# Kernel optimization log

Hardware: AMD Instinct MI355X
Metric: run time of the kernel (lower is better)

## Reference

```python
import jax, jax.numpy as jnp
import numpy as np

B, M, N, D = 16, 1024, 1024, 512
DIST_THRESH = 0.3
NUM_SINK = 8


def setup_inputs() -> dict:
    key = jax.random.key(0)
    k1, k2, k3, k4 = jax.random.split(key, 4)
    return {
        "tra_feats": jax.random.normal(k1, (B, M, D), jnp.float32),
        "det_feats": jax.random.normal(k2, (B, N, D), jnp.float32),
        "tra_loc": jax.random.uniform(k3, (B, M, 2), jnp.float32),
        "det_loc": jax.random.uniform(k4, (B, N, 2), jnp.float32),
        "alpha": jnp.ones((1,), jnp.float32),
        "eplison": jnp.zeros((1,), jnp.float32),
    }


def _sinkhorn(C, log_a, log_b, lambd, num_sink):
    # log-domain unrolled Sinkhorn: P_ij = exp(log_p), marginals a (rows), b (cols)
    log_p = -C / lambd
    def step(lp, _):
        lp = lp - (jax.nn.logsumexp(lp, axis=-1, keepdims=True) - log_a[:, None])
        lp = lp - (jax.nn.logsumexp(lp, axis=-2, keepdims=True) - log_b[None, :])
        return lp, None
    log_p, _ = jax.lax.scan(step, log_p, None, length=num_sink)
    # final row normalization (standard unrolled-sinkhorn convention)
    log_p = log_p - (jax.nn.logsumexp(log_p, axis=-1, keepdims=True) - log_a[:, None])
    return jnp.exp(log_p)


def _per_graph(tf, df, tl, dl, alpha, lambd):
    n1 = jnp.linalg.norm(tf, axis=-1, keepdims=True)          # [M,1]
    n2 = jnp.linalg.norm(df, axis=-1, keepdims=True)          # [N,1]
    d2 = jnp.sum((tl[:, None, :] - dl[None, :, :]) ** 2, -1)  # [M,N] squared cdist
    mask = (jnp.sqrt(d2) <= DIST_THRESH).astype(tf.dtype)
    corr = (tf @ df.T) / (n1 * n2.T) * mask                   # masked cosine similarity
    m, n = corr.shape
    # augment with dustbin row/col filled with learnable alpha
    top = jnp.concatenate([corr, jnp.full((m, 1), alpha, corr.dtype)], axis=1)
    bot = jnp.full((1, n + 1), alpha, corr.dtype)
    couplings = jnp.concatenate([top, bot], axis=0)           # [M+1, N+1]
    norm = 1.0 / (m + n)
    a_aug = jnp.full((m + 1,), norm, corr.dtype).at[-1].set(norm * n)
    b_aug = jnp.full((n + 1,), norm, corr.dtype).at[-1].set(norm * m)
    p = _sinkhorn(1.0 - couplings, jnp.log(a_aug), jnp.log(b_aug), lambd, NUM_SINK)
    return p * (m + n)


def reference(tra_feats, det_feats, tra_loc, det_loc, alpha, eplison):
    a = alpha[0]
    lambd = jnp.exp(eplison[0]) + 0.03
    f = jax.vmap(lambda tf, df, tl, dl: _per_graph(tf, df, tl, dl, a, lambd))
    return f(tra_feats, det_feats, tra_loc, det_loc)   # [B, M+1, N+1]
```

## Files before the change

### kernel.cpp

```cpp
#include <hip/hip_runtime.h>
#include <math.h>

#define B_ 16
#define M_ 1024
#define N_ 1024
#define D_ 512
#define MP1 1025
#define NP1 1025
#define NUM_SINK 8
#define BK 64
#define SSTR 1024
#define VSTR 1028
#define LOG_NORM (-7.6246189861593985f)
#define LOG_HALF (-0.6931471805599453f)

typedef __attribute__((ext_vector_type(8))) short bf16x8;
typedef __attribute__((ext_vector_type(4))) float f32x4;
typedef __attribute__((ext_vector_type(8))) _Float16 h16x8;

__device__ inline short f2bf(float x) {
    unsigned u = __builtin_bit_cast(unsigned, x);
    u = (u + 0x7FFFu + ((u >> 16) & 1u)) >> 16;
    return (short)u;
}

__device__ inline void gload16(const void* g, void* l) {
    __builtin_amdgcn_global_load_lds(
        (const __attribute__((address_space(1))) unsigned int*)g,
        (__attribute__((address_space(3))) unsigned int*)l, 16, 0, 0);
}

template<bool PRE>
__global__ __launch_bounds__(256) void norms_kernel_t(
    const float* __restrict__ tf, const float* __restrict__ df,
    float* __restrict__ inv1, float* __restrict__ inv2,
    unsigned short* __restrict__ tfh, unsigned short* __restrict__ dfh)
{
    int w = (blockIdx.x * 256 + threadIdx.x) >> 6;
    int lane = threadIdx.x & 63;
    if (w >= B_ * 2048) return;
    int b = w >> 11;
    int rr = w & 2047;
    const float* src;
    float* dst = nullptr;
    unsigned short* dsth = nullptr;
    if (rr < M_) { src = tf + ((size_t)b * M_ + rr) * D_;
                   if (!PRE) dst = inv1 + b * M_ + rr;
                   if (PRE)  dsth = tfh + ((size_t)b * M_ + rr) * D_; }
    else         { src = df + ((size_t)b * N_ + (rr - M_)) * D_;
                   if (!PRE) dst = inv2 + b * N_ + (rr - M_);
                   if (PRE)  dsth = dfh + ((size_t)b * N_ + (rr - M_)) * D_; }
    float4 x = *(const float4*)(src + lane * 4);
    float4 y = *(const float4*)(src + 256 + lane * 4);
    float ss = x.x*x.x + x.y*x.y + x.z*x.z + x.w*x.w
             + y.x*y.x + y.y*y.y + y.z*y.z + y.w*y.w;
    #pragma unroll
    for (int o = 32; o; o >>= 1) ss += __shfl_xor(ss, o);
    if (PRE) {
        float rn = rsqrtf(ss);
        ushort4 hx, hy;
        hx.x = (unsigned short)f2bf(x.x*rn); hx.y = (unsigned short)f2bf(x.y*rn);
        hx.z = (unsigned short)f2bf(x.z*rn); hx.w = (unsigned short)f2bf(x.w*rn);
        hy.x = (unsigned short)f2bf(y.x*rn); hy.y = (unsigned short)f2bf(y.y*rn);
        hy.z = (unsigned short)f2bf(y.z*rn); hy.w = (unsigned short)f2bf(y.w*rn);
        *(ushort4*)(dsth + lane * 4) = hx;
        *(ushort4*)(dsth + 256 + lane * 4) = hy;
    } else {
        if (lane == 0) *dst = 1.0f / sqrtf(ss);
    }
}

template<int MODE>
__global__ __launch_bounds__(256) void gemm_s_kernel(
    const void* __restrict__ A, const void* __restrict__ Bm,
    const float* __restrict__ tl, const float* __restrict__ dl,
    const float* __restrict__ inv1, const float* __restrict__ inv2,
    const float* __restrict__ eps_p, void* __restrict__ Sout)
{
    __shared__ __align__(16) unsigned short As[128 * BK];
    __shared__ __align__(16) unsigned short Bs[128 * BK];

    int flat = blockIdx.x;
    int swz = (flat & 7) * 128 + (flat >> 3);
    int jb = swz & 7, ib = (swz >> 3) & 7;
    int b  = swz >> 6;
    int i0 = ib * 128;
    int j0 = jb * 128;

    int tid  = threadIdx.x;
    int lane = tid & 63;
    int w    = tid >> 6;
    int wm   = w >> 1, wn = w & 1;

    f32x4 acc[4][4] = {};

    if constexpr (MODE == 2) {
        const unsigned short* Ah = (const unsigned short*)A  + (size_t)b * M_ * D_;
        const unsigned short* Bh = (const unsigned short*)Bm + (size_t)b * N_ * D_;
        int gcol = ((lane & 7) ^ (lane >> 3)) << 3;
        int rloc = lane >> 3;
        for (int k0 = 0; k0 < D_; k0 += BK) {
            #pragma unroll
            for (int c = 0; c < 4; ++c) {
                int r = (w * 4 + c) * 8 + rloc;
                gload16(Ah + (size_t)(i0 + r) * D_ + k0 + gcol,
                        (char*)As + (w * 4 + c) * 1024 + lane * 16);
                gload16(Bh + (size_t)(j0 + r) * D_ + k0 + gcol,
                        (char*)Bs + (w * 4 + c) * 1024 + lane * 16);
            }
            __syncthreads();
            #pragma unroll
            for (int ks = 0; ks < 2; ++ks) {
                int kb = ks * 64 + ((lane >> 4) << 4);
                bf16x8 af[4], bfr[4];
                #pragma unroll
                for (int m = 0; m < 4; ++m) {
                    int ra = wm * 64 + m * 16 + (lane & 15);
                    af[m] = *(const bf16x8*)((const char*)As + ra * 128 + (kb ^ ((ra & 7) << 4)));
                    int rb = wn * 64 + m * 16 + (lane & 15);
                    bfr[m] = *(const bf16x8*)((const char*)Bs + rb * 128 + (kb ^ ((rb & 7) << 4)));
                }
                #pragma unroll
                for (int m = 0; m < 4; ++m)
                    #pragma unroll
                    for (int n = 0; n < 4; ++n)
                        acc[m][n] = __builtin_amdgcn_mfma_f32_16x16x32_bf16(af[m], bfr[n], acc[m][n], 0, 0, 0);
            }
            __syncthreads();
        }
    } else {
        const float* Ab = (const float*)A  + (size_t)b * M_ * D_;
        const float* Bb = (const float*)Bm + (size_t)b * N_ * D_;
        int seg   = tid & 7;
        int rbase = tid >> 3;
        for (int k0 = 0; k0 < D_; k0 += BK) {
            #pragma unroll
            for (int rr = 0; rr < 4; ++rr) {
                int r = rbase + rr * 32;
                int colx = (seg * 16) ^ ((r & 7) << 4);
                {
                    const float* pa = Ab + (size_t)(i0 + r) * D_ + k0 + seg * 8;
                    float4 a0 = *(const float4*)pa;
                    float4 a1 = *(const float4*)(pa + 4);
                    bf16x8 hv;
                    hv[0] = f2bf(a0.x); hv[1] = f2bf(a0.y); hv[2] = f2bf(a0.z); hv[3] = f2bf(a0.w);
                    hv[4] = f2bf(a1.x); hv[5] = f2bf(a1.y); hv[6] = f2bf(a1.z); hv[7] = f2bf(a1.w);
                    *(bf16x8*)((char*)As + r * 128 + colx) = hv;
                }
                {
                    const float* pb = Bb + (size_t)(j0 + r) * D_ + k0 + seg * 8;
                    float4 b0 = *(const float4*)pb;
                    float4 b1 = *(const float4*)(pb + 4);
                    bf16x8 hv;
                    hv[0] = f2bf(b0.x); hv[1] = f2bf(b0.y); hv[2] = f2bf(b0.z); hv[3] = f2bf(b0.w);
                    hv[4] = f2bf(b1.x); hv[5] = f2bf(b1.y); hv[6] = f2bf(b1.z); hv[7] = f2bf(b1.w);
                    *(bf16x8*)((char*)Bs + r * 128 + colx) = hv;
                }
            }
            __syncthreads();
            #pragma unroll
            for (int ks = 0; ks < 2; ++ks) {
                int kb = ks * 64 + ((lane >> 4) << 4);
                bf16x8 af[4], bfr[4];
                #pragma unroll
                for (int m = 0; m < 4; ++m) {
                    int ra = wm * 64 + m * 16 + (lane & 15);
                    af[m] = *(const bf16x8*)((const char*)As + ra * 128 + (kb ^ ((ra & 7) << 4)));
                    int rb = wn * 64 + m * 16 + (lane & 15);
                    bfr[m] = *(const bf16x8*)((const char*)Bs + rb * 128 + (kb ^ ((rb & 7) << 4)));
                }
                #pragma unroll
                for (int m = 0; m < 4; ++m)
                    #pragma unroll
                    for (int n = 0; n < 4; ++n)
                        acc[m][n] = __builtin_amdgcn_mfma_f32_16x16x32_bf16(af[m], bfr[n], acc[m][n], 0, 0, 0);
            }
            __syncthreads();
        }
    }

    float lam = __expf(eps_p[0]) + 0.03f;
    float inv_lam = 1.0f / lam;
    int crow0 = i0 + wm * 64;
    int ccol0 = j0 + wn * 64;
    int rlane = lane >> 4;
    int clane = lane & 15;

    float invb_[4], dlx_[4], dly_[4];
    #pragma unroll
    for (int n = 0; n < 4; ++n) {
        int j = ccol0 + n * 16 + clane;
        if (MODE != 2) invb_[n] = inv2[b * N_ + j];
        dlx_[n]  = dl[((size_t)b * N_ + j) * 2 + 0];
        dly_[n]  = dl[((size_t)b * N_ + j) * 2 + 1];
    }
    #pragma unroll
    for (int m = 0; m < 4; ++m) {
        #pragma unroll
        for (int reg = 0; reg < 4; ++reg) {
            int i = crow0 + m * 16 + rlane * 4 + reg;
            float inva = (MODE != 2) ? inv1[b * M_ + i] : 1.0f;
            float tlx  = tl[((size_t)b * M_ + i) * 2 + 0];
            float tly  = tl[((size_t)b * M_ + i) * 2 + 1];
            #pragma unroll
            for (int n = 0; n < 4; ++n) {
                float cosv = (MODE == 2) ? acc[m][n][reg]
                                         : acc[m][n][reg] * inva * invb_[n];
                float dx = tlx - dlx_[n];
                float dy = tly - dly_[n];
                float msk = (dx * dx + dy * dy <= 0.09f) ? 1.0f : 0.0f;
                float val = (cosv * msk - 1.0f) * inv_lam;
                int col = ccol0 + n * 16 + clane;
                if (MODE >= 1) {
                    _Float16* Srow = (_Float16*)Sout + ((size_t)b * M_ + i) * SSTR;
                    Srow[col] = (_Float16)val;
                } else {
                    float* Srow = (float*)Sout + ((size_t)b * MP1 + i) * NP1;
                    Srow[col] = val;
                }
            }
        }
    }
}

__global__ __launch_bounds__(256) void init_hv(
    float* __restrict__ v, float* __restrict__ sums_p)
{
    int t = blockIdx.x * 256 + threadIdx.x;
    if (t < B_ * VSTR) v[t] = 0.f;
    int u2 = t - B_ * VSTR;
    if (u2 >= 0 && u2 < 2 * B_ * 17) {
        int p = u2 / (B_ * 17), s = u2 % 17;
        sums_p[u2] = (p == 0 && s == 0) ? 1025.0f : 0.f;
    }
}

__global__ __launch_bounds__(256) void rowcol32(
    const _Float16* __restrict__ Sh, const float* __restrict__ v,
    float* __restrict__ ps,
    const float* __restrict__ alpha_p, const float* __restrict__ eps_p)
{
    int blk = blockIdx.x;
    int b = blk >> 5, k = blk & 31;
    int tid = threadIdx.x, lane = tid & 63, w = tid >> 6;

    __shared__ float red[4][64][17];

    const float* vb = v + (size_t)b * VSTR;
    float vreg[16];
    {
        float4 v0 = *(const float4*)(vb + lane * 8);
        float4 v1 = *(const float4*)(vb + lane * 8 + 4);
        float4 v2 = *(const float4*)(vb + 512 + lane * 8);
        float4 v3 = *(const float4*)(vb + 512 + lane * 8 + 4);
        vreg[0]=v0.x; vreg[1]=v0.y; vreg[2]=v0.z; vreg[3]=v0.w;
        vreg[4]=v1.x; vreg[5]=v1.y; vreg[6]=v1.z; vreg[7]=v1.w;
        vreg[8]=v2.x; vreg[9]=v2.y; vreg[10]=v2.z; vreg[11]=v2.w;
        vreg[12]=v3.x; vreg[13]=v3.y; vreg[14]=v3.z; vreg[15]=v3.w;
    }
    float lam = __expf(eps_p[0]) + 0.03f;
    float s_a = (alpha_p[0] - 1.0f) / lam;
    float et16c = __expf(s_a + vb[1024]);

    const _Float16* Sb = Sh + ((size_t)b << 20);
    int rbase = k * 32 + w * 8;

    float creg[16] = {};
    float sum_scale = 0.f;

    #pragma unroll
    for (int g = 0; g < 2; ++g) {
        h16x8 h0[4], h1[4];
        #pragma unroll
        for (int rr = 0; rr < 4; ++rr) {
            const _Float16* row = Sb + (size_t)(rbase + g * 4 + rr) * SSTR;
            h0[rr] = *(const h16x8*)(row + lane * 8);
            h1[rr] = *(const h16x8*)(row + 512 + lane * 8);
        }
        #pragma unroll
        for (int rr = 0; rr < 4; ++rr) {
            float et[16];
            float rs = 0.f;
            #pragma unroll
            for (int e = 0; e < 8; ++e) { et[e] = __expf((float)h0[rr][e] + vreg[e]); rs += et[e]; }
            #pragma unroll
            for (int e = 0; e < 8; ++e) { et[8+e] = __expf((float)h1[rr][e] + vreg[8+e]); rs += et[8+e]; }
            #pragma unroll
            for (int o = 32; o; o >>= 1) rs += __shfl_xor(rs, o);
            rs += et16c;
            float scale = (1.0f / 2048.0f) / rs;
            #pragma unroll
            for (int e = 0; e < 16; ++e) creg[e] += et[e] * scale;
            sum_scale += scale;
        }
    }

    #pragma unroll
    for (int e = 0; e < 16; ++e) red[w][lane][e] = creg[e];
    if (lane == 0) red[w][0][16] = sum_scale;
    __syncthreads();

    float* pso = ps + (size_t)(k * 16 + b) * 1025;
    for (int j = tid; j < 1024; j += 256) {
        int lane_j = (j & 511) >> 3;
        int e_j    = ((j >> 9) << 3) | (j & 7);
        pso[j] = red[0][lane_j][e_j] + red[1][lane_j][e_j]
               + red[2][lane_j][e_j] + red[3][lane_j][e_j];
    }
    if (tid == 0)
        pso[1024] = et16c * (red[0][0][16] + red[1][0][16] + red[2][0][16] + red[3][0][16]);
}

__global__ __launch_bounds__(256) void colpass32(
    const float* __restrict__ ps, float* __restrict__ v,
    float* __restrict__ sums_p, int it)
{
    int gw = blockIdx.x * 4 + (threadIdx.x >> 6);
    int lane = threadIdx.x & 63;
    if (gw >= B_ * 17) return;
    int b = gw / 17, seg = gw % 17;
    int j = seg * 64 + lane;
    int par = it & 1;
    float sum_old = 0.f;
    #pragma unroll
    for (int s = 0; s < 17; ++s) sum_old += sums_p[par * (B_ * 17) + b * 17 + s];
    float ev = 0.f;
    if (j <= 1024) {
        size_t vidx = (size_t)b * VSTR + j;
        float vj = v[vidx];
        const float* pp = ps + (size_t)b * 1025 + j;
        float cs = 0.f;
        #pragma unroll 8
        for (int c = 0; c < 32; ++c) cs += pp[(size_t)c * (16 * 1025)];
        cs += 0.5f * __expf(vj) / sum_old;
        float lb = (j == 1024) ? LOG_HALF : LOG_NORM;
        float vn = vj + lb - __logf(cs);
        v[vidx] = vn;
        ev = __expf(vn);
    }
    #pragma unroll
    for (int o = 32; o; o >>= 1) ev += __shfl_xor(ev, o);
    if (lane == 0) sums_p[(par ^ 1) * (B_ * 17) + b * 17 + seg] = ev;
}

__global__ __launch_bounds__(256) void final32(
    const _Float16* __restrict__ Sh, const float* __restrict__ v,
    const float* __restrict__ sums_p,
    const float* __restrict__ alpha_p, const float* __restrict__ eps_p,
    float* __restrict__ out)
{
    int blk = blockIdx.x;
    int tid = threadIdx.x, lane = tid & 63, w = tid >> 6;

    if (blk >= 512) {
        int gw = (blk - 512) * 4 + w;
        if (gw >= B_ * 17) return;
        int b = gw / 17, seg = gw % 17, j = seg * 64 + lane;
        if (j > 1024) return;
        float sumv = 0.f;
        int par = NUM_SINK & 1;
        #pragma unroll
        for (int s = 0; s < 17; ++s) sumv += sums_p[par * (B_ * 17) + b * 17 + s];
        out[((size_t)b * MP1 + 1024) * NP1 + j] = __expf(v[(size_t)b * VSTR + j]) * 1024.0f / sumv;
        return;
    }

    int b = blk >> 5, k = blk & 31;
    const float* vb = v + (size_t)b * VSTR;
    float vreg[16];
    {
        float4 v0 = *(const float4*)(vb + lane * 8);
        float4 v1 = *(const float4*)(vb + lane * 8 + 4);
        float4 v2 = *(const float4*)(vb + 512 + lane * 8);
        float4 v3 = *(const float4*)(vb + 512 + lane * 8 + 4);
        vreg[0]=v0.x; vreg[1]=v0.y; vreg[2]=v0.z; vreg[3]=v0.w;
        vreg[4]=v1.x; vreg[5]=v1.y; vreg[6]=v1.z; vreg[7]=v1.w;
        vreg[8]=v2.x; vreg[9]=v2.y; vreg[10]=v2.z; vreg[11]=v2.w;
        vreg[12]=v3.x; vreg[13]=v3.y; vreg[14]=v3.z; vreg[15]=v3.w;
    }
    float lam = __expf(eps_p[0]) + 0.03f;
    float s_a = (alpha_p[0] - 1.0f) / lam;
    float et16c = __expf(s_a + vb[1024]);

    const _Float16* Sb = Sh + ((size_t)b << 20);
    int rbase = k * 32 + w * 8;

    #pragma unroll
    for (int g = 0; g < 2; ++g) {
        h16x8 h0[4], h1[4];
        #pragma unroll
        for (int rr = 0; rr < 4; ++rr) {
            const _Float16* row = Sb + (size_t)(rbase + g * 4 + rr) * SSTR;
            h0[rr] = *(const h16x8*)(row + lane * 8);
            h1[rr] = *(const h16x8*)(row + 512 + lane * 8);
        }
        #pragma unroll
        for (int rr = 0; rr < 4; ++rr) {
            int r = rbase + g * 4 + rr;
            float et[16];
            float rs = 0.f;
            #pragma unroll
            for (int e = 0; e < 8; ++e) { et[e] = __expf((float)h0[rr][e] + vreg[e]); rs += et[e]; }
            #pragma unroll
            for (int e = 0; e < 8; ++e) { et[8+e] = __expf((float)h1[rr][e] + vreg[8+e]); rs += et[8+e]; }
            #pragma unroll
            for (int o = 32; o; o >>= 1) rs += __shfl_xor(rs, o);
            rs += et16c;
            float sc = 1.0f / rs;
            float* orow = out + ((size_t)b * MP1 + r) * NP1;
            float4 o0 = {et[0]*sc,  et[1]*sc,  et[2]*sc,  et[3]*sc};
            float4 o1 = {et[4]*sc,  et[5]*sc,  et[6]*sc,  et[7]*sc};
            float4 o2 = {et[8]*sc,  et[9]*sc,  et[10]*sc, et[11]*sc};
            float4 o3 = {et[12]*sc, et[13]*sc, et[14]*sc, et[15]*sc};
            *(float4*)(orow + lane * 8)           = o0;
            *(float4*)(orow + lane * 8 + 4)       = o1;
            *(float4*)(orow + 512 + lane * 8)     = o2;
            *(float4*)(orow + 512 + lane * 8 + 4) = o3;
            if (lane == 0) orow[1024] = et16c * sc;
        }
    }
}


__global__ __launch_bounds__(256) void fill_edges_f32(
    float* __restrict__ Sout, const float* __restrict__ alpha_p, const float* __restrict__ eps_p)
{
    int t = blockIdx.x * 256 + threadIdx.x;
    if (t >= B_ * (NP1 + M_)) return;
    int b = t / (NP1 + M_), r = t % (NP1 + M_);
    float lam = expf(eps_p[0]) + 0.03f;
    float s = (alpha_p[0] - 1.0f) / lam;
    size_t idx;
    if (r < NP1) idx = ((size_t)b * MP1 + M_) * NP1 + r;
    else         idx = ((size_t)b * MP1 + (r - NP1)) * NP1 + N_;
    Sout[idx] = s;
}

__global__ __launch_bounds__(256) void row_pass_kernel(
    const float* __restrict__ S, const float* __restrict__ v, float* __restrict__ u)
{
    int w = (blockIdx.x * 256 + threadIdx.x) >> 6;
    int lane = threadIdx.x & 63;
    if (w >= B_ * MP1) return;
    int b = w / MP1, i = w % MP1;
    const float* row = S + ((size_t)b * MP1 + i) * NP1;
    const float* vb = v + b * NP1;
    float sm = 0.f;
    #pragma unroll
    for (int q = 0; q < 17; ++q) {
        int j = lane + q * 64;
        if (j < NP1) sm += expf(row[j] + vb[j]);
    }
    #pragma unroll
    for (int o = 32; o; o >>= 1) sm += __shfl_xor(sm, o);
    if (lane == 0) {
        float la = (i == M_) ? LOG_HALF : LOG_NORM;
        u[b * MP1 + i] = la - logf(sm);
    }
}

__global__ __launch_bounds__(256) void col_pass1_kernel(
    const float* __restrict__ S, const float* __restrict__ u,
    float* __restrict__ pm, float* __restrict__ ps)
{
    int j = blockIdx.x * 256 + threadIdx.x;
    int b = blockIdx.z;
    int i0 = blockIdx.y * 128;
    int i1 = min(i0 + 128, MP1);
    if (j >= NP1) return;
    const float* p  = S + ((size_t)b * MP1 + i0) * NP1 + j;
    const float* ub = u + b * MP1;
    float sm = 0.f;
    for (int i = i0; i < i1; ++i) {
        sm += expf(*p + ub[i]);
        p += NP1;
    }
    int idx = (blockIdx.y * B_ + b) * NP1 + j;
    pm[idx] = 0.f;
    ps[idx] = sm;
}

__global__ __launch_bounds__(256) void col_pass2_kernel(
    const float* __restrict__ pm, const float* __restrict__ ps, float* __restrict__ v)
{
    int j = blockIdx.x * 256 + threadIdx.x;
    int b = blockIdx.y;
    if (j >= NP1) return;
    float Ssum = 0.f;
    #pragma unroll
    for (int c = 0; c < 9; ++c) Ssum += ps[(c * B_ + b) * NP1 + j];
    float lb = (j == N_) ? LOG_HALF : LOG_NORM;
    v[b * NP1 + j] = lb - logf(Ssum);
}

__global__ __launch_bounds__(256) void row_final_kernel(
    float* __restrict__ S, const float* __restrict__ v)
{
    int w = (blockIdx.x * 256 + threadIdx.x) >> 6;
    int lane = threadIdx.x & 63;
    if (w >= B_ * MP1) return;
    int b = w / MP1, i = w % MP1;
    float* row = S + ((size_t)b * MP1 + i) * NP1;
    const float* vb = v + b * NP1;
    float et[17];
    float sm = 0.f;
    #pragma unroll
    for (int q = 0; q < 17; ++q) {
        int j = lane + q * 64;
        float e = 0.f;
        if (j < NP1) e = expf(row[j] + vb[j]);
        et[q] = e;
        sm += e;
    }
    #pragma unroll
    for (int o = 32; o; o >>= 1) sm += __shfl_xor(sm, o);
    float A = (i == M_) ? 0.5f : (1.0f / 2048.0f);
    float scale = (A / sm) * 2048.0f;
    #pragma unroll
    for (int q = 0; q < 17; ++q) {
        int j = lane + q * 64;
        if (j < NP1) row[j] = et[q] * scale;
    }
}

__global__ __launch_bounds__(256) void zero_kernel(float* __restrict__ p, int n)
{
    int i = blockIdx.x * 256 + threadIdx.x;
    if (i < n) p[i] = 0.f;
}

extern "C" void kernel_launch(void* const* d_in, const int* in_sizes, int n_in,
                              void* d_out, int out_size, void* d_ws, size_t ws_size,
                              hipStream_t stream)
{
    const float* tf    = (const float*)d_in[0];
    const float* df    = (const float*)d_in[1];
    const float* tl    = (const float*)d_in[2];
    const float* dl    = (const float*)d_in[3];
    const float* alpha = (const float*)d_in[4];
    const float* eps   = (const float*)d_in[5];
    float* out = (float*)d_out;

    const size_t bf_one   = (size_t)B_ * M_ * D_ * 2;
    const size_t sh_bytes = (size_t)B_ * M_ * SSTR * 2;
    const size_t vf       = (size_t)B_ * VSTR;
    const size_t sums_f   = 2 * B_ * 17;
    const size_t invs_f   = (size_t)B_ * M_ * 2;
    const size_t need_pre = 2 * bf_one + sh_bytes + (vf + sums_f) * 4 + 512;
    const size_t need_mid = sh_bytes + (vf + sums_f + invs_f) * 4 + 512;

    int initblocks = (int)((vf + sums_f + 255) / 256);

    if (ws_size >= need_pre) {
        unsigned short* tfh = (unsigned short*)d_ws;
        unsigned short* dfh = tfh + (size_t)B_ * M_ * D_;
        _Float16* Sh = (_Float16*)((char*)d_ws + 2 * bf_one);
        float* fbase = (float*)((char*)d_ws + ((2 * bf_one + sh_bytes + 255) & ~(size_t)255));
        float* v      = fbase;
        float* sums_p = v + vf;
        float* ps     = out;

        init_hv<<<initblocks, 256, 0, stream>>>(v, sums_p);
        norms_kernel_t<true><<<(B_ * 2048) / 4, 256, 0, stream>>>(tf, df, nullptr, nullptr, tfh, dfh);
        gemm_s_kernel<2><<<1024, 256, 0, stream>>>(tfh, dfh, tl, dl, nullptr, nullptr, eps, Sh);

        for (int it = 0; it < NUM_SINK; ++it) {
            rowcol32<<<512, 256, 0, stream>>>(Sh, v, ps, alpha, eps);
            colpass32<<<68, 256, 0, stream>>>(ps, v, sums_p, it);
        }
        final32<<<580, 256, 0, stream>>>(Sh, v, sums_p, alpha, eps, out);
    } else if (ws_size >= need_mid) {
        _Float16* Sh = (_Float16*)d_ws;
        float* fbase = (float*)((char*)d_ws + ((sh_bytes + 255) & ~(size_t)255));
        float* inv1   = fbase;
        float* inv2   = inv1 + B_ * M_;
        float* v      = inv2 + B_ * N_;
        float* sums_p = v + vf;
        float* ps     = out;

        init_hv<<<initblocks, 256, 0, stream>>>(v, sums_p);
        norms_kernel_t<false><<<(B_ * 2048) / 4, 256, 0, stream>>>(tf, df, inv1, inv2, nullptr, nullptr);
        gemm_s_kernel<1><<<1024, 256, 0, stream>>>(tf, df, tl, dl, inv1, inv2, eps, Sh);

        for (int it = 0; it < NUM_SINK; ++it) {
            rowcol32<<<512, 256, 0, stream>>>(Sh, v, ps, alpha, eps);
            colpass32<<<68, 256, 0, stream>>>(ps, v, sums_p, it);
        }
        final32<<<580, 256, 0, stream>>>(Sh, v, sums_p, alpha, eps, out);
    } else {
        float* S = out;
        float* ws = (float*)d_ws;
        float* inv1 = ws;
        float* inv2 = inv1 + B_ * M_;
        float* u    = inv2 + B_ * N_;
        float* v    = u + B_ * MP1;
        float* pm   = v + B_ * NP1;
        float* ps   = pm + 9 * B_ * NP1;

        zero_kernel<<<(B_ * NP1 + 255) / 256, 256, 0, stream>>>(v, B_ * NP1);
        norms_kernel_t<false><<<(B_ * 2048) / 4, 256, 0, stream>>>(tf, df, inv1, inv2, nullptr, nullptr);
        gemm_s_kernel<0><<<1024, 256, 0, stream>>>(tf, df, tl, dl, inv1, inv2, eps, S);
        fill_edges_f32<<<(B_ * (NP1 + M_) + 255) / 256, 256, 0, stream>>>(S, alpha, eps);

        int rowblocks = (B_ * MP1 + 3) / 4;
        for (int it = 0; it < NUM_SINK; ++it) {
            row_pass_kernel<<<rowblocks, 256, 0, stream>>>(S, v, u);
            col_pass1_kernel<<<dim3(5, 9, 16), 256, 0, stream>>>(S, u, pm, ps);
            col_pass2_kernel<<<dim3(5, 16), 256, 0, stream>>>(pm, ps, v);
        }
        row_final_kernel<<<rowblocks, 256, 0, stream>>>(S, v);
    }
}
```

Baseline: 168.7 us.

## Double-buffer GEMM LDS tiles, fold init into norms kernel, batch row loads

The bf16 GEMM path now keeps two LDS buffers and issues the next K-tile's global-to-LDS loads before computing on the current one, so load latency overlaps with MFMA work. The separate init kernel is dropped and its zeroing of v and sums is done by block 0 of the norms kernel, removing one launch. The row/column pass now loads all 8 rows up front instead of in two groups of 4, and the mask/scale arithmetic is folded into fmas. Doubling LDS per block and raising register use may lower occupancy.

```diff
diff --git a/kernel.cpp b/kernel.cpp
--- a/kernel.cpp
+++ b/kernel.cpp
@@ -34,8 +34,20 @@
 __global__ __launch_bounds__(256) void norms_kernel_t(
     const float* __restrict__ tf, const float* __restrict__ df,
     float* __restrict__ inv1, float* __restrict__ inv2,
-    unsigned short* __restrict__ tfh, unsigned short* __restrict__ dfh)
-{
+    unsigned short* __restrict__ tfh, unsigned short* __restrict__ dfh,
+    float* __restrict__ v, float* __restrict__ sums_p)
+{
+    if (PRE && blockIdx.x == 0) {
+        const int nv = B_ * VSTR, ns = 2 * B_ * 17;
+        for (int t = threadIdx.x; t < nv + ns; t += 256) {
+            if (t < nv) v[t] = 0.f;
+            else {
+                int u2 = t - nv;
+                int p = u2 / (B_ * 17), s = u2 % 17;
+                sums_p[u2] = (p == 0 && s == 0) ? 1025.0f : 0.f;
+            }
+        }
+    }
     int w = (blockIdx.x * 256 + threadIdx.x) >> 6;
     int lane = threadIdx.x & 63;
     if (w >= B_ * 2048) return;
@@ -77,8 +89,8 @@
     const float* __restrict__ inv1, const float* __restrict__ inv2,
     const float* __restrict__ eps_p, void* __restrict__ Sout)
 {
-    __shared__ __align__(16) unsigned short As[128 * BK];
-    __shared__ __align__(16) unsigned short Bs[128 * BK];
+    __shared__ __align__(16) unsigned short As[2][128 * BK];
+    __shared__ __align__(16) unsigned short Bs[2][128 * BK];
 
     int flat = blockIdx.x;
     int swz = (flat & 7) * 128 + (flat >> 3);
@@ -99,16 +111,23 @@
         const unsigned short* Bh = (const unsigned short*)Bm + (size_t)b * N_ * D_;
         int gcol = ((lane & 7) ^ (lane >> 3)) << 3;
         int rloc = lane >> 3;
-        for (int k0 = 0; k0 < D_; k0 += BK) {
+
+        auto stage = [&](int k0, int buf) {
             #pragma unroll
             for (int c = 0; c < 4; ++c) {
                 int r = (w * 4 + c) * 8 + rloc;
                 gload16(Ah + (size_t)(i0 + r) * D_ + k0 + gcol,
-                        (char*)As + (w * 4 + c) * 1024 + lane * 16);
+                        (char*)As[buf] + (w * 4 + c) * 1024 + lane * 16);
                 gload16(Bh + (size_t)(j0 + r) * D_ + k0 + gcol,
-                        (char*)Bs + (w * 4 + c) * 1024 + lane * 16);
+                        (char*)Bs[buf] + (w * 4 + c) * 1024 + lane * 16);
             }
-            __syncthreads();
+        };
+
+        stage(0, 0);
+        __syncthreads();
+        int cur = 0;
+        for (int t = 0; t < D_ / BK; ++t) {
+            if (t < D_ / BK - 1) stage((t + 1) * BK, cur ^ 1);
             #pragma unroll
             for (int ks = 0; ks < 2; ++ks) {
                 int kb = ks * 64 + ((lane >> 4) << 4);
@@ -116,9 +135,9 @@
                 #pragma unroll
                 for (int m = 0; m < 4; ++m) {
                     int ra = wm * 64 + m * 16 + (lane & 15);
-                    af[m] = *(const bf16x8*)((const char*)As + ra * 128 + (kb ^ ((ra & 7) << 4)));
+                    af[m] = *(const bf16x8*)((const char*)As[cur] + ra * 128 + (kb ^ ((ra & 7) << 4)));
                     int rb = wn * 64 + m * 16 + (lane & 15);
-                    bfr[m] = *(const bf16x8*)((const char*)Bs + rb * 128 + (kb ^ ((rb & 7) << 4)));
+                    bfr[m] = *(const bf16x8*)((const char*)Bs[cur] + rb * 128 + (kb ^ ((rb & 7) << 4)));
                 }
                 #pragma unroll
                 for (int m = 0; m < 4; ++m)
@@ -127,6 +146,7 @@
                         acc[m][n] = __builtin_amdgcn_mfma_f32_16x16x32_bf16(af[m], bfr[n], acc[m][n], 0, 0, 0);
             }
             __syncthreads();
+            cur ^= 1;
         }
     } else {
         const float* Ab = (const float*)A  + (size_t)b * M_ * D_;
@@ -145,7 +165,7 @@
                     bf16x8 hv;
                     hv[0] = f2bf(a0.x); hv[1] = f2bf(a0.y); hv[2] = f2bf(a0.z); hv[3] = f2bf(a0.w);
                     hv[4] = f2bf(a1.x); hv[5] = f2bf(a1.y); hv[6] = f2bf(a1.z); hv[7] = f2bf(a1.w);
-                    *(bf16x8*)((char*)As + r * 128 + colx) = hv;
+                    *(bf16x8*)((char*)As[0] + r * 128 + colx) = hv;
                 }
                 {
                     const float* pb = Bb + (size_t)(j0 + r) * D_ + k0 + seg * 8;
@@ -154,7 +174,7 @@
                     bf16x8 hv;
                     hv[0] = f2bf(b0.x); hv[1] = f2bf(b0.y); hv[2] = f2bf(b0.z); hv[3] = f2bf(b0.w);
                     hv[4] = f2bf(b1.x); hv[5] = f2bf(b1.y); hv[6] = f2bf(b1.z); hv[7] = f2bf(b1.w);
-                    *(bf16x8*)((char*)Bs + r * 128 + colx) = hv;
+                    *(bf16x8*)((char*)Bs[0] + r * 128 + colx) = hv;
                 }
             }
             __syncthreads();
@@ -165,9 +185,9 @@
                 #pragma unroll
                 for (int m = 0; m < 4; ++m) {
                     int ra = wm * 64 + m * 16 + (lane & 15);
-                    af[m] = *(const bf16x8*)((const char*)As + ra * 128 + (kb ^ ((ra & 7) << 4)));
+                    af[m] = *(const bf16x8*)((const char*)As[0] + ra * 128 + (kb ^ ((ra & 7) << 4)));
                     int rb = wn * 64 + m * 16 + (lane & 15);
-                    bfr[m] = *(const bf16x8*)((const char*)Bs + rb * 128 + (kb ^ ((rb & 7) << 4)));
+                    bfr[m] = *(const bf16x8*)((const char*)Bs[0] + rb * 128 + (kb ^ ((rb & 7) << 4)));
                 }
                 #pragma unroll
                 for (int m = 0; m < 4; ++m)
@@ -208,8 +228,8 @@
                                          : acc[m][n][reg] * inva * invb_[n];
                 float dx = tlx - dlx_[n];
                 float dy = tly - dly_[n];
-                float msk = (dx * dx + dy * dy <= 0.09f) ? 1.0f : 0.0f;
-                float val = (cosv * msk - 1.0f) * inv_lam;
+                float mi = (fmaf(dx, dx, dy * dy) <= 0.09f) ? inv_lam : 0.0f;
+                float val = fmaf(cosv, mi, -inv_lam);
                 int col = ccol0 + n * 16 + clane;
                 if (MODE >= 1) {
                     _Float16* Srow = (_Float16*)Sout + ((size_t)b * M_ + i) * SSTR;
@@ -265,34 +285,32 @@
     const _Float16* Sb = Sh + ((size_t)b << 20);
     int rbase = k * 32 + w * 8;
 
+    h16x8 h0[8], h1[8];
+    #pragma unroll
+    for (int rr = 0; rr < 8; ++rr) {
+        const _Float16* row = Sb + (size_t)(rbase + rr) * SSTR;
+        h0[rr] = *(const h16x8*)(row + lane * 8);
+        h1[rr] = *(const h16x8*)(row + 512 + lane * 8);
+    }
+
     float creg[16] = {};
     float sum_scale = 0.f;
 
     #pragma unroll
-    for (int g = 0; g < 2; ++g) {
-        h16x8 h0[4], h1[4];
-        #pragma unroll
-        for (int rr = 0; rr < 4; ++rr) {
-            const _Float16* row = Sb + (size_t)(rbase + g * 4 + rr) * SSTR;
-            h0[rr] = *(const h16x8*)(row + lane * 8);
-            h1[rr] = *(const h16x8*)(row + 512 + lane * 8);
-        }
-        #pragma unroll
-        for (int rr = 0; rr < 4; ++rr) {
-            float et[16];
-            float rs = 0.f;
-            #pragma unroll
-            for (int e = 0; e < 8; ++e) { et[e] = __expf((float)h0[rr][e] + vreg[e]); rs += et[e]; }
-            #pragma unroll
-            for (int e = 0; e < 8; ++e) { et[8+e] = __expf((float)h1[rr][e] + vreg[8+e]); rs += et[8+e]; }
-            #pragma unroll
-            for (int o = 32; o; o >>= 1) rs += __shfl_xor(rs, o);
-            rs += et16c;
-            float scale = (1.0f / 2048.0f) / rs;
-            #pragma unroll
-            for (int e = 0; e < 16; ++e) creg[e] += et[e] * scale;
-            sum_scale += scale;
-        }
+    for (int rr = 0; rr < 8; ++rr) {
+        float et[16];
+        float rs = 0.f;
+        #pragma unroll
+        for (int e = 0; e < 8; ++e) { et[e] = __expf((float)h0[rr][e] + vreg[e]); rs += et[e]; }
+        #pragma unroll
+        for (int e = 0; e < 8; ++e) { et[8+e] = __expf((float)h1[rr][e] + vreg[8+e]); rs += et[8+e]; }
+        #pragma unroll
+        for (int o = 32; o; o >>= 1) rs += __shfl_xor(rs, o);
+        rs += et16c;
+        float scale = (1.0f / 2048.0f) / rs;
+        #pragma unroll
+        for (int e = 0; e < 16; ++e) creg[e] += et[e] * scale;
+        sum_scale += scale;
     }
 
     #pragma unroll
@@ -560,8 +578,7 @@
         float* sums_p = v + vf;
         float* ps     = out;
 
-        init_hv<<<initblocks, 256, 0, stream>>>(v, sums_p);
-        norms_kernel_t<true><<<(B_ * 2048) / 4, 256, 0, stream>>>(tf, df, nullptr, nullptr, tfh, dfh);
+        norms_kernel_t<true><<<(B_ * 2048) / 4, 256, 0, stream>>>(tf, df, nullptr, nullptr, tfh, dfh, v, sums_p);
         gemm_s_kernel<2><<<1024, 256, 0, stream>>>(tfh, dfh, tl, dl, nullptr, nullptr, eps, Sh);
 
         for (int it = 0; it < NUM_SINK; ++it) {
@@ -579,7 +596,7 @@
         float* ps     = out;
 
         init_hv<<<initblocks, 256, 0, stream>>>(v, sums_p);
-        norms_kernel_t<false><<<(B_ * 2048) / 4, 256, 0, stream>>>(tf, df, inv1, inv2, nullptr, nullptr);
+        norms_kernel_t<false><<<(B_ * 2048) / 4, 256, 0, stream>>>(tf, df, inv1, inv2, nullptr, nullptr, nullptr, nullptr);
         gemm_s_kernel<1><<<1024, 256, 0, stream>>>(tf, df, tl, dl, inv1, inv2, eps, Sh);
 
         for (int it = 0; it < NUM_SINK; ++it) {
@@ -598,7 +615,7 @@
         float* ps   = pm + 9 * B_ * NP1;
 
         zero_kernel<<<(B_ * NP1 + 255) / 256, 256, 0, stream>>>(v, B_ * NP1);
-        norms_kernel_t<false><<<(B_ * 2048) / 4, 256, 0, stream>>>(tf, df, inv1, inv2, nullptr, nullptr);
+        norms_kernel_t<false><<<(B_ * 2048) / 4, 256, 0, stream>>>(tf, df, inv1, inv2, nullptr, nullptr, nullptr, nullptr);
         gemm_s_kernel<0><<<1024, 256, 0, stream>>>(tf, df, tl, dl, inv1, inv2, eps, S);
         fill_edges_f32<<<(B_ * (NP1 + M_) + 255) / 256, 256, 0, stream>>>(S, alpha, eps);
 
```

Result: faster. 161.8 us (-4.1%).
